# Optimization experiments

Hardware: AMD Instinct MI355X
Metric: run time of the kernel (lower is better)

The kernel has to match this reference:

```python
import jax, jax.numpy as jnp
import numpy as np

B, L, E, V = 256, 256, 100, 100000  # trees, leaves per tree, embed_size, vocab
T = L - 1                           # compose steps per tree (left fold)


def setup_inputs() -> dict:
    key = jax.random.key(0)
    k1, k2, k3, k4 = jax.random.split(key, 4)
    token_ids = jax.random.randint(k1, (B, L), 0, V)
    # Left-fold composition plan shared across the batch (buffer layout:
    # slots [0,L) hold leaf embeddings, slot L+t holds the step-t result).
    # step 0: compose(leaf0, leaf1); step t>0: compose(result_{t-1}, leaf_{t+1})
    comp_left = jnp.concatenate([jnp.array([0], jnp.int32),
                                 (L + jnp.arange(T - 1)).astype(jnp.int32)])
    comp_left = jnp.broadcast_to(comp_left, (B, T))
    comp_right = jnp.broadcast_to(jnp.arange(1, L, dtype=jnp.int32), (B, T))
    embeddings = jax.random.normal(k2, (V, E), jnp.float32)
    W1 = jax.random.normal(k3, (E, 2 * E), jnp.float32) * (1.0 / np.sqrt(2 * E))
    b1 = jnp.zeros((E,), jnp.float32)
    W2 = jax.random.normal(k4, (1, E), jnp.float32) * (1.0 / np.sqrt(E))
    b2 = jnp.zeros((1,), jnp.float32)
    return dict(token_ids=token_ids, comp_left=comp_left, comp_right=comp_right,
                embeddings=embeddings, W1=W1, b1=b1, W2=W2, b2=b2)


def reference(token_ids, comp_left, comp_right, embeddings, W1, b1, W2, b2):
    leaf = embeddings[token_ids]                                  # [B, L, E]
    buf = jnp.concatenate([leaf, jnp.zeros((B, T, E), leaf.dtype)], axis=1)  # [B, L+T, E]
    bidx = jnp.arange(B)

    def step(buf, xs):
        t, li, ri = xs                                            # li, ri: [B]
        left = buf[bidx, li]                                      # [B, E]
        right = buf[bidx, ri]                                     # [B, E]
        ab = jnp.concatenate([left, right], axis=-1)              # [B, 2E]
        out = jnp.tanh(ab @ W1.T + b1)                            # compose
        buf = buf.at[bidx, L + t].set(out)
        return buf, None

    xs = (jnp.arange(T), comp_left.T, comp_right.T)
    buf, _ = jax.lax.scan(step, buf, xs)
    root = buf[:, L + T - 1]                                      # [B, E]
    return jax.nn.sigmoid(root @ W2.T + b2)                       # [B, 1]
```

## Files before the change

### kernel.cpp

```cpp
#include <hip/hip_runtime.h>
#include <math.h>


#define Bc 256
#define Lc 256
#define Ec 100
#define Tc 255
#define W1cols 200

#define RL(v, k) __int_as_float(__builtin_amdgcn_readlane(__float_as_int(v), (k)))
#define RF(x)    __builtin_amdgcn_readfirstlane(x)

#define REP25(X) X(0) X(1) X(2) X(3) X(4) X(5) X(6) X(7) X(8) X(9) X(10) X(11) X(12) \
                 X(13) X(14) X(15) X(16) X(17) X(18) X(19) X(20) X(21) X(22) X(23) X(24)
#define DECLWC(j) float wA##j, wB##j;
#define LOADWC(j) { wA##j = rowA[j]; wB##j = rowB[j]; }
#define CM2(a,b) { const float ra_ = RL(sv,(a)), rb_ = RL(sv,(b)); \
    accA0 = fmaf(ra_, wA##a, accA0); accB0 = fmaf(ra_, wB##a, accB0); \
    accA1 = fmaf(rb_, wA##b, accA1); accB1 = fmaf(rb_, wB##b, accB1); }
#define CM1(a) { const float ra_ = RL(sv,(a)); \
    accA0 = fmaf(ra_, wA##a, accA0); accB0 = fmaf(ra_, wB##a, accB0); }
#define CMALL CM2(0,1) CM2(2,3) CM2(4,5) CM2(6,7) CM2(8,9) CM2(10,11) CM2(12,13) \
              CM2(14,15) CM2(16,17) CM2(18,19) CM2(20,21) CM2(22,23) CM1(24)

#define REP100(X) \
 X(0) X(1) X(2) X(3) X(4) X(5) X(6) X(7) X(8) X(9) X(10) X(11) X(12) X(13) X(14) X(15) \
 X(16) X(17) X(18) X(19) X(20) X(21) X(22) X(23) X(24) X(25) X(26) X(27) X(28) X(29) X(30) X(31) \
 X(32) X(33) X(34) X(35) X(36) X(37) X(38) X(39) X(40) X(41) X(42) X(43) X(44) X(45) X(46) X(47) \
 X(48) X(49) X(50) X(51) X(52) X(53) X(54) X(55) X(56) X(57) X(58) X(59) X(60) X(61) X(62) X(63) \
 X(64) X(65) X(66) X(67) X(68) X(69) X(70) X(71) X(72) X(73) X(74) X(75) X(76) X(77) X(78) X(79) \
 X(80) X(81) X(82) X(83) X(84) X(85) X(86) X(87) X(88) X(89) X(90) X(91) X(92) X(93) X(94) X(95) \
 X(96) X(97) X(98) X(99)
#define DECLW(k) float w##k;
#define SRCP(k) RL((k) < 64 ? vA : vB, (k) < 64 ? (k) : (k) - 64)
#define G8(S,a,b,c,d,e,f,g,h2) { \
    const float r0_=S(a), r1_=S(b), r2_=S(c), r3_=S(d), \
                r4_=S(e), r5_=S(f), r6_=S(g), r7_=S(h2); \
    acc0 = fmaf(r0_, w##a, acc0); acc1 = fmaf(r1_, w##b, acc1); \
    acc2 = fmaf(r2_, w##c, acc2); acc3 = fmaf(r3_, w##d, acc3); \
    acc0 = fmaf(r4_, w##e, acc0); acc1 = fmaf(r5_, w##f, acc1); \
    acc2 = fmaf(r6_, w##g, acc2); acc3 = fmaf(r7_, w##h2, acc3); }
#define G2(S,a,b) { const float r0_=S(a), r1_=S(b); \
    acc0 = fmaf(r0_, w##a, acc0); acc1 = fmaf(r1_, w##b, acc1); }
#define CHUNKA(S) G8(S,0,1,2,3,4,5,6,7) G8(S,8,9,10,11,12,13,14,15) \
                  G8(S,16,17,18,19,20,21,22,23) G8(S,24,25,26,27,28,29,30,31) \
                  G8(S,32,33,34,35,36,37,38,39) G8(S,40,41,42,43,44,45,46,47) G2(S,48,49)
#define CHUNKB(S) G8(S,50,51,52,53,54,55,56,57) G8(S,58,59,60,61,62,63,64,65) \
                  G8(S,66,67,68,69,70,71,72,73) G8(S,74,75,76,77,78,79,80,81) \
                  G8(S,82,83,84,85,86,87,88,89) G8(S,90,91,92,93,94,95,96,97) G2(S,98,99)

__device__ __noinline__ float slow_dot(const float* rp, const float* wr) {
    float a0 = 0.f, a1 = 0.f, a2 = 0.f, a3 = 0.f;
    for (int qq = 0; qq < 25; ++qq) {
        float4 h4 = *(const float4*)(rp + 4 * qq);
        float4 w4 = *(const float4*)(wr + 4 * qq);
        a0 = fmaf(w4.x, h4.x, a0); a1 = fmaf(w4.y, h4.y, a1);
        a2 = fmaf(w4.z, h4.z, a2); a3 = fmaf(w4.w, h4.w, a3);
    }
    return (a0 + a1) + (a2 + a3);
}

__global__ __launch_bounds__(512, 2)
void fused(const int* __restrict__ token_ids,
           const int* __restrict__ comp_left,
           const int* __restrict__ comp_right,
           const float* __restrict__ emb,
           const float* __restrict__ W1,
           const float* __restrict__ b1,
           const float* __restrict__ W2,
           const float* __restrict__ b2,
           float* __restrict__ out)
{
    const int b    = blockIdx.x;
    const int tid  = threadIdx.x;
    const int wv   = tid >> 6;
    const int l    = tid & 63;
    const bool cons = (wv < 4);
    const int q    = wv & 3;
    const int lc   = (l < 50) ? l : 49;

    __shared__ float hist[Tc * Ec];
    __shared__ float cring[4][Ec];
    __shared__ float part[2][4][Ec];
    __shared__ int2  ccS[Tc];
    __shared__ int   tokRS[Tc], tokLS[Tc];
    __shared__ float red[4];

    for (int i = tid; i < Tc; i += 512) {
        const int cl = comp_left [b * Tc + i];
        const int cr = comp_right[b * Tc + i];
        ccS[i]   = make_int2(cl, cr);
        tokRS[i] = (cr < Lc) ? token_ids[b * Lc + cr] : -1;
        tokLS[i] = (cl < Lc) ? token_ids[b * Lc + cl] : -1;
    }

    const float* rowA = W1 + (size_t)lc * W1cols + 25 * q;
    const float* rowB = W1 + (size_t)(lc + 50) * W1cols + 25 * q;
    REP25(DECLWC)
    const int pw   = wv - 4;
    const int pp_  = pw >> 1;
    const int pm   = pw & 1;
    const int prow = 50 * pm + lc;
    const float* wrow = W1 + (size_t)prow * W1cols + Ec;
    REP100(DECLW)
    float b1e = 0.f;
    if (cons) { REP25(LOADWC) }
    else {
#define LOADW(k) w##k = wrow[k];
        REP100(LOADW)
#undef LOADW
        b1e = b1[prow];
    }

    __syncthreads();

    float vh = 0.f;
    int2  cc = make_int2(0, 0);
    float pvA = 0.f, pvB = 0.f;
    float nA = 0.f, nB = 0.f;
    float acc0 = 0.f, acc1 = 0.f, acc2 = 0.f, acc3 = 0.f;

#define PISSUE(tnext) { \
    const int tk_ = ((tnext) < Tc) ? RF(tokRS[(tnext)]) : -1;               \
    if (tk_ >= 0) { const float* g_ = emb + (size_t)tk_ * Ec;               \
        nA = g_[l]; nB = (l < 36) ? g_[64 + l] : 0.f; }                     \
    else { nA = 0.f; nB = 0.f; } }

    if (cons) {
        cc = ccS[0];
    } else {
        const int tk = RF(tokRS[pp_]);
        float pA = 0.f, pB = 0.f;
        if (tk >= 0) {
            const float* g = emb + (size_t)tk * Ec;
            pA = g[l];
            if (l < 36) pB = g[64 + l];
        }
        acc0 = b1e;
        { const float vA = pA, vB = pB; CHUNKA(SRCP) CHUNKB(SRCP) }
        if (l < 50) cring[pp_ & 3][prow] = (acc0 + acc1) + (acc2 + acc3);
        PISSUE(pp_ + 2)
    }

#define BARRIER asm volatile("s_waitcnt lgkmcnt(0)\n\ts_barrier" ::: "memory");

#define TICK(I, PPc, PAR)                                                     \
{                                                                             \
    const int i_ = (I);                                                       \
    if (cons) {                                                               \
        const int tc = i_ - 1;                                                \
        if (tc >= 0) {                                                        \
            __builtin_amdgcn_s_setprio(1);                                    \
            const int li = RF(cc.x);                                          \
            const int ri = RF(cc.y);                                          \
            float cv = 0.f;                                                   \
            if (l < 25) cv = cring[tc & 3][25 * q + l];                       \
            float sv = 0.f;                                                   \
            if (tc >= 1 && li == Lc + tc - 1) {                               \
                sv = vh;                              \
            } else if (li >= Lc) {                                            \
                const int n = li - Lc;                                        \
                if (n < tc && l < 25) sv = hist[n * Ec + 25 * q + l];         \
            } else {                                                          \
                const int tl = RF(tokLS[tc]);                                 \
                if (tl >= 0 && l < 25) sv = emb[(size_t)tl * Ec + 25 * q + l];\
            }                                                                 \
            float accA0 = 0.f, accA1 = 0.f, accB0 = 0.f, accB1 = 0.f;         \
            CMALL                                                             \
            if (l < 50) {                                                     \
                part[PPc][q][l]      = accA0 + accA1;                         \
                part[PPc][q][l + 50] = accB0 + accB1;                         \
            }                                                                 \
            BARRIER                                                           \
            if (l < 25) {                                                     \
                const int r = 25 * q + l;                                     \
                float x = ((part[PPc][0][r] + part[PPc][1][r]) +              \
                           (part[PPc][2][r] + part[PPc][3][r])) + cv;         \
                if (ri >= Lc) {                                               \
                    const int n = ri - Lc;                                    \
                    if (n < tc) x += slow_dot(&hist[n * Ec],                  \
                                              W1 + (size_t)r * W1cols + Ec);  \
                }                                                             \
                const float u = __expf(2.f * x);                              \
                vh = 1.f - 2.f / (u + 1.f);         \
                hist[tc * Ec + r] = vh;               \
            }                                                                 \
            __builtin_amdgcn_s_setprio(0);                                    \
            if (tc + 1 < Tc) cc = ccS[tc + 1];                                \
        } else {                                                              \
            BARRIER                                                           \
        }                                                                     \
    } else {                                                                  \
        if (pp_ == (PAR)) {                        \
            const int t = i_ + 2;                                             \
            if (t < Tc) {                                                     \
                pvA = nA; pvB = nB;             \
                PISSUE(t + 2)                                                 \
                acc0 = b1e; acc1 = 0.f; acc2 = 0.f; acc3 = 0.f;               \
                { const float vA = pvA, vB = pvB; CHUNKA(SRCP) }              \
            }                                                                 \
        } else {                                  \
            const int t = i_ + 1;                                             \
            if (t >= pp_ + 2 && t < Tc) {                                     \
                { const float vA = pvA, vB = pvB; CHUNKB(SRCP) }              \
                if (l < 50) cring[t & 3][prow] = (acc0 + acc1) + (acc2 + acc3);\
            }                                                                 \
        }                                                                     \
        BARRIER                                                               \
    }                                                                         \
}

    #pragma unroll 1
    for (int i2 = 0; i2 < 256; i2 += 2) {
        TICK(i2,     1, 0)
        TICK(i2 + 1, 0, 1)
    }
#undef TICK
#undef PISSUE
#undef BARRIER

    if (cons) {
        float pv = 0.f;
        if (l < 25) pv = W2[25 * q + l] * vh;
        #pragma unroll
        for (int off = 32; off > 0; off >>= 1) pv += __shfl_down(pv, off, 64);
        if (l == 0) red[q] = pv;
    }
    __syncthreads();
    if (tid == 0)
        out[b] = 1.f / (1.f + __expf(-((red[0] + red[1]) + (red[2] + red[3]) + b2[0])));
}

extern "C" void kernel_launch(void* const* d_in, const int* in_sizes, int n_in,
                              void* d_out, int out_size, void* d_ws, size_t ws_size,
                              hipStream_t stream) {
    const int*   token_ids  = (const int*)  d_in[0];
    const int*   comp_left  = (const int*)  d_in[1];
    const int*   comp_right = (const int*)  d_in[2];
    const float* emb        = (const float*)d_in[3];
    const float* W1         = (const float*)d_in[4];
    const float* b1         = (const float*)d_in[5];
    const float* W2         = (const float*)d_in[6];
    const float* b2         = (const float*)d_in[7];
    float*       out        = (float*)d_out;

    fused<<<Bc, 512, 0, stream>>>(token_ids, comp_left, comp_right,
                                  emb, W1, b1, W2, b2, out);
}
```

Baseline: 140.7 us.

## Split producer leaf-projection across four K-quarter waves like consumers

Producer waves now each handle a 25-wide K slice of the right-leaf embedding for all 100 outputs, using the same CMALL readlane pattern as the consumers. Each therefore holds 50 weights instead of 100 and computes every step rather than alternating chunk A and B on paired waves. Partial sums go to an 8-deep cpart ring laid out [row][quarter] so the consumer can read them with one float4. The part buffer is transposed the same way. This cuts the producer's per-step readlane chain and register pressure, but uses more shared memory.

Result: faster. 129.7 us (-7.8%).

```diff
diff --git a/kernel.cpp b/kernel.cpp
--- a/kernel.cpp
+++ b/kernel.cpp
@@ -22,32 +22,6 @@
     accA0 = fmaf(ra_, wA##a, accA0); accB0 = fmaf(ra_, wB##a, accB0); }
 #define CMALL CM2(0,1) CM2(2,3) CM2(4,5) CM2(6,7) CM2(8,9) CM2(10,11) CM2(12,13) \
               CM2(14,15) CM2(16,17) CM2(18,19) CM2(20,21) CM2(22,23) CM1(24)
-
-#define REP100(X) \
- X(0) X(1) X(2) X(3) X(4) X(5) X(6) X(7) X(8) X(9) X(10) X(11) X(12) X(13) X(14) X(15) \
- X(16) X(17) X(18) X(19) X(20) X(21) X(22) X(23) X(24) X(25) X(26) X(27) X(28) X(29) X(30) X(31) \
- X(32) X(33) X(34) X(35) X(36) X(37) X(38) X(39) X(40) X(41) X(42) X(43) X(44) X(45) X(46) X(47) \
- X(48) X(49) X(50) X(51) X(52) X(53) X(54) X(55) X(56) X(57) X(58) X(59) X(60) X(61) X(62) X(63) \
- X(64) X(65) X(66) X(67) X(68) X(69) X(70) X(71) X(72) X(73) X(74) X(75) X(76) X(77) X(78) X(79) \
- X(80) X(81) X(82) X(83) X(84) X(85) X(86) X(87) X(88) X(89) X(90) X(91) X(92) X(93) X(94) X(95) \
- X(96) X(97) X(98) X(99)
-#define DECLW(k) float w##k;
-#define SRCP(k) RL((k) < 64 ? vA : vB, (k) < 64 ? (k) : (k) - 64)
-#define G8(S,a,b,c,d,e,f,g,h2) { \
-    const float r0_=S(a), r1_=S(b), r2_=S(c), r3_=S(d), \
-                r4_=S(e), r5_=S(f), r6_=S(g), r7_=S(h2); \
-    acc0 = fmaf(r0_, w##a, acc0); acc1 = fmaf(r1_, w##b, acc1); \
-    acc2 = fmaf(r2_, w##c, acc2); acc3 = fmaf(r3_, w##d, acc3); \
-    acc0 = fmaf(r4_, w##e, acc0); acc1 = fmaf(r5_, w##f, acc1); \
-    acc2 = fmaf(r6_, w##g, acc2); acc3 = fmaf(r7_, w##h2, acc3); }
-#define G2(S,a,b) { const float r0_=S(a), r1_=S(b); \
-    acc0 = fmaf(r0_, w##a, acc0); acc1 = fmaf(r1_, w##b, acc1); }
-#define CHUNKA(S) G8(S,0,1,2,3,4,5,6,7) G8(S,8,9,10,11,12,13,14,15) \
-                  G8(S,16,17,18,19,20,21,22,23) G8(S,24,25,26,27,28,29,30,31) \
-                  G8(S,32,33,34,35,36,37,38,39) G8(S,40,41,42,43,44,45,46,47) G2(S,48,49)
-#define CHUNKB(S) G8(S,50,51,52,53,54,55,56,57) G8(S,58,59,60,61,62,63,64,65) \
-                  G8(S,66,67,68,69,70,71,72,73) G8(S,74,75,76,77,78,79,80,81) \
-                  G8(S,82,83,84,85,86,87,88,89) G8(S,90,91,92,93,94,95,96,97) G2(S,98,99)
 
 __device__ __noinline__ float slow_dot(const float* rp, const float* wr) {
     float a0 = 0.f, a1 = 0.f, a2 = 0.f, a3 = 0.f;
@@ -80,8 +54,8 @@
     const int lc   = (l < 50) ? l : 49;
 
     __shared__ float hist[Tc * Ec];
-    __shared__ float cring[4][Ec];
-    __shared__ float part[2][4][Ec];
+    __shared__ __align__(16) float part[2][Ec][4];
+    __shared__ __align__(16) float cpart[8][Ec][4];
     __shared__ int2  ccS[Tc];
     __shared__ int   tokRS[Tc], tokLS[Tc];
     __shared__ float red[4];
@@ -94,52 +68,39 @@
         tokLS[i] = (cl < Lc) ? token_ids[b * Lc + cl] : -1;
     }
 
-    const float* rowA = W1 + (size_t)lc * W1cols + 25 * q;
-    const float* rowB = W1 + (size_t)(lc + 50) * W1cols + 25 * q;
+    const int kofs = (cons ? 0 : Ec) + 25 * q;
+    const float* rowA = W1 + (size_t)lc * W1cols + kofs;
+    const float* rowB = W1 + (size_t)(lc + 50) * W1cols + kofs;
     REP25(DECLWC)
-    const int pw   = wv - 4;
-    const int pp_  = pw >> 1;
-    const int pm   = pw & 1;
-    const int prow = 50 * pm + lc;
-    const float* wrow = W1 + (size_t)prow * W1cols + Ec;
-    REP100(DECLW)
-    float b1e = 0.f;
-    if (cons) { REP25(LOADWC) }
-    else {
-#define LOADW(k) w##k = wrow[k];
-        REP100(LOADW)
-#undef LOADW
-        b1e = b1[prow];
-    }
+    REP25(LOADWC)
+    const float b1eA = (!cons && q == 0) ? b1[lc] : 0.f;
+    const float b1eB = (!cons && q == 0) ? b1[lc + 50] : 0.f;
 
     __syncthreads();
 
     float vh = 0.f;
     int2  cc = make_int2(0, 0);
-    float pvA = 0.f, pvB = 0.f;
-    float nA = 0.f, nB = 0.f;
-    float acc0 = 0.f, acc1 = 0.f, acc2 = 0.f, acc3 = 0.f;
-
-#define PISSUE(tnext) { \
-    const int tk_ = ((tnext) < Tc) ? RF(tokRS[(tnext)]) : -1;               \
-    if (tk_ >= 0) { const float* g_ = emb + (size_t)tk_ * Ec;               \
-        nA = g_[l]; nB = (l < 36) ? g_[64 + l] : 0.f; }                     \
-    else { nA = 0.f; nB = 0.f; } }
+    float vA0 = 0.f, vA1 = 0.f;
+    int   tk0 = -1, tk1 = -1;
 
     if (cons) {
         cc = ccS[0];
     } else {
-        const int tk = RF(tokRS[pp_]);
-        float pA = 0.f, pB = 0.f;
-        if (tk >= 0) {
-            const float* g = emb + (size_t)tk * Ec;
-            pA = g[l];
-            if (l < 36) pB = g[64 + l];
+        for (int t = 0; t < 2; ++t) {
+            const int tk = RF(tokRS[t]);
+            float sv = 0.f;
+            if (tk >= 0 && l < 25) sv = emb[(size_t)tk * Ec + 25 * q + l];
+            float accA0 = b1eA, accA1 = 0.f, accB0 = b1eB, accB1 = 0.f;
+            if (tk >= 0) { CMALL }
+            if (l < 50) {
+                cpart[t][lc][q]      = accA0 + accA1;
+                cpart[t][lc + 50][q] = accB0 + accB1;
+            }
         }
-        acc0 = b1e;
-        { const float vA = pA, vB = pB; CHUNKA(SRCP) CHUNKB(SRCP) }
-        if (l < 50) cring[pp_ & 3][prow] = (acc0 + acc1) + (acc2 + acc3);
-        PISSUE(pp_ + 2)
+        tk0 = (2 < Tc) ? RF(tokRS[2]) : -1;
+        if (tk0 >= 0 && l < 25) vA0 = emb[(size_t)tk0 * Ec + 25 * q + l];
+        tk1 = (3 < Tc) ? RF(tokRS[3]) : -1;
+        if (tk1 >= 0 && l < 25) vA1 = emb[(size_t)tk1 * Ec + 25 * q + l];
     }
 
 #define BARRIER asm volatile("s_waitcnt lgkmcnt(0)\n\ts_barrier" ::: "memory");
@@ -153,8 +114,6 @@
             __builtin_amdgcn_s_setprio(1);                                    \
             const int li = RF(cc.x);                                          \
             const int ri = RF(cc.y);                                          \
-            float cv = 0.f;                                                   \
-            if (l < 25) cv = cring[tc & 3][25 * q + l];                       \
             float sv = 0.f;                                                   \
             if (tc >= 1 && li == Lc + tc - 1) {                               \
                 sv = vh;                              \
@@ -168,14 +127,16 @@
             float accA0 = 0.f, accA1 = 0.f, accB0 = 0.f, accB1 = 0.f;         \
             CMALL                                                             \
             if (l < 50) {                                                     \
-                part[PPc][q][l]      = accA0 + accA1;                         \
-                part[PPc][q][l + 50] = accB0 + accB1;                         \
+                part[PPc][lc][q]      = accA0 + accA1;                        \
+                part[PPc][lc + 50][q] = accB0 + accB1;                        \
             }                                                                 \
             BARRIER                                                           \
             if (l < 25) {                                                     \
                 const int r = 25 * q + l;                                     \
-                float x = ((part[PPc][0][r] + part[PPc][1][r]) +              \
-                           (part[PPc][2][r] + part[PPc][3][r])) + cv;         \
+                const float4 p4 = *(const float4*)&part[PPc][r][0];           \
+                const float4 c4 = *(const float4*)&cpart[tc & 7][r][0];       \
+                float x = ((p4.x + p4.y) + (p4.z + p4.w)) +                   \
+                          ((c4.x + c4.y) + (c4.z + c4.w));                    \
                 if (ri >= Lc) {                                               \
                     const int n = ri - Lc;                                    \
                     if (n < tc) x += slow_dot(&hist[n * Ec],                  \
@@ -191,19 +152,20 @@
             BARRIER                                                           \
         }                                                                     \
     } else {                                                                  \
-        if (pp_ == (PAR)) {                        \
-            const int t = i_ + 2;                                             \
-            if (t < Tc) {                                                     \
-                pvA = nA; pvB = nB;             \
-                PISSUE(t + 2)                                                 \
-                acc0 = b1e; acc1 = 0.f; acc2 = 0.f; acc3 = 0.f;               \
-                { const float vA = pvA, vB = pvB; CHUNKA(SRCP) }              \
-            }                                                                 \
-        } else {                                  \
-            const int t = i_ + 1;                                             \
-            if (t >= pp_ + 2 && t < Tc) {                                     \
-                { const float vA = pvA, vB = pvB; CHUNKB(SRCP) }              \
-                if (l < 50) cring[t & 3][prow] = (acc0 + acc1) + (acc2 + acc3);\
+        const int t = i_ + 2;                                                 \
+        if (t < Tc) {                                                         \
+            const float sv  = (PAR) ? vA1 : vA0;      \
+            const int   tkc = (PAR) ? tk1 : tk0;                              \
+            const int   tn  = t + 2;                    \
+            const int tknew = (tn < Tc) ? RF(tokRS[tn]) : -1;                 \
+            float nv = 0.f;                                                   \
+            if (tknew >= 0 && l < 25) nv = emb[(size_t)tknew * Ec + 25 * q + l];\
+            if (PAR) { vA1 = nv; tk1 = tknew; } else { vA0 = nv; tk0 = tknew; }\
+            float accA0 = b1eA, accA1 = 0.f, accB0 = b1eB, accB1 = 0.f;       \
+            if (tkc >= 0) { CMALL }                                           \
+            if (l < 50) {                                                     \
+                cpart[t & 7][lc][q]      = accA0 + accA1;                     \
+                cpart[t & 7][lc + 50][q] = accB0 + accB1;                     \
             }                                                                 \
         }                                                                     \
         BARRIER                                                               \
@@ -216,7 +178,6 @@
         TICK(i2 + 1, 0, 1)
     }
 #undef TICK
-#undef PISSUE
 #undef BARRIER
 
     if (cons) {
```
